# Kernel tuning notes

Measured on AMD Instinct MI355X. Metric: run time of the kernel, lower is better.

The kernel has to match this reference:

```python
import jax, jax.numpy as jnp
import numpy as np

N = 100000        # nodes
E = 1600000       # edges
D = 128           # feature dim (all layers)
G = 128           # graphs
C = 10            # num_classes
L = 3             # conv layers
EPS = 1e-5
SLOPE = 0.03


def setup_inputs() -> dict:
    key = jax.random.key(0)
    ks = jax.random.split(key, 12)
    x = jax.random.normal(ks[0], (N, D), dtype=jnp.float32)
    edge_index = jax.random.randint(ks[1], (2, E), 0, N, dtype=jnp.int64)
    batch = jnp.sort(jax.random.randint(ks[2], (N,), 0, G, dtype=jnp.int64))
    s = 1.0 / np.sqrt(D)
    Wc = jax.random.uniform(ks[3], (L, D, D), jnp.float32, -s, s)
    bc = jax.random.uniform(ks[4], (L, D), jnp.float32, -s, s)
    bn_gamma = jnp.ones((2, D), jnp.float32)
    bn_beta = jnp.zeros((2, D), jnp.float32)
    bn_mean = jax.random.normal(ks[5], (2, D), jnp.float32) * 0.1
    bn_var = jax.random.uniform(ks[6], (2, D), jnp.float32, 0.5, 1.5)
    lin_w = jax.random.uniform(ks[7], (C, D), jnp.float32, -s, s)
    lin_b = jax.random.uniform(ks[8], (C,), jnp.float32, -s, s)
    return {"x": x, "edge_index": edge_index, "batch": batch, "Wc": Wc,
            "bc": bc, "bn_gamma": bn_gamma, "bn_beta": bn_beta,
            "bn_mean": bn_mean, "bn_var": bn_var, "lin_w": lin_w, "lin_b": lin_b}


def _gcn_norm(edge_index):
    # add self-loops, compute D^{-1/2}[row] * D^{-1/2}[col] (PyG gcn_norm)
    loops = jnp.arange(N, dtype=edge_index.dtype)
    row = jnp.concatenate([edge_index[0], loops])
    col = jnp.concatenate([edge_index[1], loops])
    deg = jax.ops.segment_sum(jnp.ones_like(col, dtype=jnp.float32), col, num_segments=N)
    dis = jnp.where(deg > 0, jax.lax.rsqrt(deg), 0.0)
    return row, col, dis[row] * dis[col]


def reference(x, edge_index, batch, Wc, bc, bn_gamma, bn_beta, bn_mean, bn_var, lin_w, lin_b):
    row, col, norm = _gcn_norm(edge_index)
    h = x
    for i in range(L):
        h = h @ Wc[i]                                          # linear transform [N, D]
        msg = h[row] * norm[:, None]                           # gather + normalize [E+N, D]
        h = jax.ops.segment_sum(msg, col, num_segments=N) + bc[i]
        if i < 2:  # batchnorm only for i < len(batchnorms)-1 (eval mode, running stats)
            h = (h - bn_mean[i]) * jax.lax.rsqrt(bn_var[i] + EPS) * bn_gamma[i] + bn_beta[i]
        h = jnp.where(h > 0, h, SLOPE * h)                     # LeakyReLU(0.03)
    # global mean pool over graphs
    counts = jax.ops.segment_sum(jnp.ones((N,), jnp.float32), batch, num_segments=G)
    pooled = jax.ops.segment_sum(h, batch, num_segments=G) / jnp.maximum(counts, 1.0)[:, None]
    # dropout is identity in eval; final linear head
    return pooled @ lin_w.T + lin_b                            # [G, C]
```

## Files before the change

### kernel.cpp

```cpp
#include <hip/hip_runtime.h>
#include <hip/hip_bf16.h>

#define NN 100000
#define EE 1600000
#define DD 128
#define GG 128
#define CC 10
#define NPB 256
#define NB 391
#define SCAP 5120
#define VPT 16
#define CPAD 32
#define PPN 64

typedef __attribute__((ext_vector_type(8))) short bf16x8;
typedef __attribute__((ext_vector_type(4))) float f32x4;
typedef unsigned int u32;

__device__ inline float blo(u32 u) { return __uint_as_float(u << 16); }
__device__ inline float bhi(u32 u) { return __uint_as_float(u & 0xffff0000u); }
__device__ inline u32 bpack(float x, float y) {
    u32 bx = __float_as_uint(x);
    u32 by = __float_as_uint(y);
    bx = (bx + 0x7fffu + ((bx >> 16) & 1u)) >> 16;
    by = (by + 0x7fffu + ((by >> 16) & 1u)) & 0xffff0000u;
    return bx | by;
}

__global__ __launch_bounds__(256) void k_bcount(const int* __restrict__ col,
                                                int* __restrict__ bhist) {
    __shared__ int lh[NB];
    int tid = threadIdx.x;
    for (int b = tid; b < NB; b += 256) lh[b] = 0;
    __syncthreads();
    int base = blockIdx.x * (256 * VPT);
#pragma unroll
    for (int j = 0; j < VPT; j++) {
        int e = base + j * 256 + tid;
        if (e < EE) atomicAdd(&lh[col[e] >> 8], 1);
    }
    __syncthreads();
    for (int b = tid; b < NB; b += 256) {
        int h = lh[b];
        if (h) atomicAdd(&bhist[b * CPAD], h);
    }
}

__global__ __launch_bounds__(512) void k_bscan(const int* __restrict__ bhist,
                                               int* __restrict__ boffs,
                                               int* __restrict__ bcur) {
    __shared__ int s[512];
    int tid = threadIdx.x;
    int c = (tid < NB) ? bhist[tid * CPAD] : 0;
    s[tid] = c;
    __syncthreads();
    for (int off = 1; off < 512; off <<= 1) {
        int v = (tid >= off) ? s[tid - off] : 0;
        __syncthreads();
        s[tid] += v;
        __syncthreads();
    }
    int excl = s[tid] - c;
    if (tid < NB) {
        boffs[tid] = excl;
        bcur[tid * CPAD] = excl;
    }
    if (tid == NB - 1) boffs[NB] = excl + c;
}

__global__ __launch_bounds__(256) void k_part(const int* __restrict__ row, const int* __restrict__ col,
                                              int* __restrict__ bcur, u32* __restrict__ pairs) {
    __shared__ int lhist[NB];
    __shared__ int gbase[NB];
    __shared__ int lcur[NB];
    int tid = threadIdx.x;
    for (int b = tid; b < NB; b += 256) lhist[b] = 0;
    __syncthreads();
    int base = blockIdx.x * (256 * VPT);
    u32 v[VPT];
    int bb[VPT];
#pragma unroll
    for (int j = 0; j < VPT; j++) {
        int e = base + j * 256 + tid;
        if (e < EE) {
            int r = row[e], c = col[e];
            v[j] = ((u32)r << 8) | (u32)(c & 255);
            bb[j] = c >> 8;
            atomicAdd(&lhist[bb[j]], 1);
        } else {
            bb[j] = -1;
        }
    }
    __syncthreads();
    for (int b = tid; b < NB; b += 256) {
        int h = lhist[b];
        gbase[b] = h ? atomicAdd(&bcur[b * CPAD], h) : 0;
        lcur[b] = 0;
    }
    __syncthreads();
#pragma unroll
    for (int j = 0; j < VPT; j++) {
        if (bb[j] >= 0) {
            int slot = gbase[bb[j]] + atomicAdd(&lcur[bb[j]], 1);
            pairs[slot] = v[j];
        }
    }
}

__global__ __launch_bounds__(256) void k_sort(const u32* __restrict__ pairs,
                                              const int* __restrict__ boffs,
                                              int* __restrict__ offs,
                                              float* __restrict__ dis,
                                              int* __restrict__ src) {
    int b = blockIdx.x;
    int tid = threadIdx.x;
    int nstart = b << 8;
    int nvalid = NN - nstart;
    if (nvalid > NPB) nvalid = NPB;
    int base = boffs[b];
    int eend = boffs[b + 1];
    int cnt = eend - base;
    __shared__ int lcnt[NPB];
    __shared__ int lscan[NPB];
    __shared__ int lcur[NPB];
    __shared__ int lsrc[SCAP];
    lcnt[tid] = 0;
    __syncthreads();
    for (int e = base + tid; e < eend; e += 256)
        atomicAdd(&lcnt[pairs[e] & 255u], 1);
    __syncthreads();
    int c = lcnt[tid];
    lscan[tid] = c;
    __syncthreads();
    for (int off = 1; off < 256; off <<= 1) {
        int v = (tid >= off) ? lscan[tid - off] : 0;
        __syncthreads();
        lscan[tid] += v;
        __syncthreads();
    }
    int excl = lscan[tid] - c;
    if (tid < nvalid) {
        offs[nstart + tid] = base + excl;
        dis[nstart + tid] = rsqrtf((float)(c + 1));
    }
    if (b == NB - 1 && tid == 255) offs[NN] = EE;
    lcur[tid] = excl;
    __syncthreads();
    if (cnt <= SCAP) {
        for (int e = base + tid; e < eend; e += 256) {
            u32 v = pairs[e];
            int slot = atomicAdd(&lcur[v & 255u], 1);
            lsrc[slot] = (int)(v >> 8);
        }
        __syncthreads();
        for (int i = tid; i < cnt; i += 256)
            src[base + i] = lsrc[i];
    } else {
        for (int e = base + tid; e < eend; e += 256) {
            u32 v = pairs[e];
            int slot = base + atomicAdd(&lcur[v & 255u], 1);
            src[slot] = (int)(v >> 8);
        }
    }
}

__global__ void k_prep(const float* __restrict__ Wc, const float* __restrict__ bc,
                       const float* __restrict__ gamma, const float* __restrict__ beta,
                       const float* __restrict__ mean, const float* __restrict__ var,
                       __hip_bfloat16* __restrict__ WT,
                       float* __restrict__ sc, float* __restrict__ tc) {
    int i = blockIdx.x * 256 + threadIdx.x;
    if (i < 3 * 128) {
        int l = i >> 7, d = i & 127;
        float s, t;
        if (l < 2) {
            float rs = rsqrtf(var[l * 128 + d] + 1e-5f);
            s = gamma[l * 128 + d] * rs;
            t = (bc[l * 128 + d] - mean[l * 128 + d]) * s + beta[l * 128 + d];
        } else {
            s = 1.f;
            t = bc[2 * 128 + d];
        }
        sc[i] = s; tc[i] = t;
    }
    if (i < 3 * 16384) {
        int l = i >> 14, r = (i >> 7) & 127, k = i & 127;
        WT[i] = __float2bfloat16(Wc[l * 16384 + k * 128 + r]);
    }
}

template <int FP32IN>
__global__ __launch_bounds__(256) void k_gemm(const void* __restrict__ Ain,
                                              const __hip_bfloat16* __restrict__ WT,
                                              const float* __restrict__ dis,
                                              __hip_bfloat16* __restrict__ Cout) {
    int wave = threadIdx.x >> 6, lane = threadIdx.x & 63;
    int lg = lane >> 4, lr = lane & 15;
    int r0w = blockIdx.x * 64 + wave * 16;
    f32x4 zero = {0.f, 0.f, 0.f, 0.f};
    f32x4 acc[8];
#pragma unroll
    for (int ct = 0; ct < 8; ct++) acc[ct] = zero;

    int arow = r0w + lr;
    if (arow > NN - 1) arow = NN - 1;

#pragma unroll
    for (int kk = 0; kk < 4; kk++) {
        bf16x8 a;
        if (FP32IN) {
            const float* ap = (const float*)Ain + (size_t)arow * 128 + kk * 32 + lg * 8;
            float4 f0 = *(const float4*)ap;
            float4 f1 = *(const float4*)(ap + 4);
            u32 t0 = bpack(f0.x, f0.y), t1 = bpack(f0.z, f0.w);
            u32 t2 = bpack(f1.x, f1.y), t3 = bpack(f1.z, f1.w);
            uint4 t = make_uint4(t0, t1, t2, t3);
            a = *(bf16x8*)&t;
        } else {
            a = *(const bf16x8*)((const __hip_bfloat16*)Ain + (size_t)arow * 128 + kk * 32 + lg * 8);
        }
#pragma unroll
        for (int ct = 0; ct < 8; ct++) {
            bf16x8 b = *(const bf16x8*)(WT + (size_t)(ct * 16 + lr) * 128 + kk * 32 + lg * 8);
            acc[ct] = __builtin_amdgcn_mfma_f32_16x16x32_bf16(a, b, acc[ct], 0, 0, 0);
        }
    }
    float dv[4];
#pragma unroll
    for (int r = 0; r < 4; r++) {
        int row = r0w + lg * 4 + r;
        dv[r] = (row < NN) ? dis[row] : 0.f;
    }
#pragma unroll
    for (int ct = 0; ct < 8; ct++) {
#pragma unroll
        for (int r = 0; r < 4; r++) {
            int row = r0w + lg * 4 + r;
            if (row < NN) Cout[(size_t)row * 128 + ct * 16 + lr] = __float2bfloat16(acc[ct][r] * dv[r]);
        }
    }
}

__global__ __launch_bounds__(256) void k_agg(const u32* __restrict__ hin,
                                             const int* __restrict__ offs,
                                             const int* __restrict__ src,
                                             const float* __restrict__ dis,
                                             const float* __restrict__ sc,
                                             const float* __restrict__ tc,
                                             u32* __restrict__ hout) {
    int node = (blockIdx.x << 2) + (threadIdx.x >> 6);
    int lane = threadIdx.x & 63;
    if (node >= NN) return;
    int e0 = __builtin_amdgcn_readfirstlane(offs[node]);
    int e1 = __builtin_amdgcn_readfirstlane(offs[node + 1]);
    u32 self = hin[(u32)node * 64u + lane];
    float a0 = blo(self), a1 = bhi(self);
    for (int e = e0; e < e1; e += 8) {
        int lim = e1 - e;
        u32 u[8];
#pragma unroll
        for (int j = 0; j < 8; j++) {
            int s = (j < lim) ? src[e + j] : node;
            u[j] = hin[(u32)s * 64u + lane];
        }
#pragma unroll
        for (int j = 0; j < 8; j++) {
            if (j < lim) { a0 += blo(u[j]); a1 += bhi(u[j]); }
        }
    }
    float dn = dis[node];
    int d0 = lane * 2;
    float r0 = (a0 * dn) * sc[d0] + tc[d0];
    float r1 = (a1 * dn) * sc[d0 + 1] + tc[d0 + 1];
    r0 = r0 > 0.f ? r0 : 0.03f * r0;
    r1 = r1 > 0.f ? r1 : 0.03f * r1;
    hout[(u32)node * 64u + lane] = bpack(r0, r1);
}

__global__ __launch_bounds__(64) void k_pool(const u32* __restrict__ h,
                                             const int* __restrict__ batch,
                                             float* __restrict__ pooled,
                                             float* __restrict__ counts) {
    int lane = threadIdx.x;
    int n0 = blockIdx.x * PPN;
    if (n0 >= NN) return;
    int n1 = n0 + PPN;
    if (n1 > NN) n1 = NN;
    float a0 = 0.f, a1 = 0.f, cnt = 0.f;
    int g = batch[n0];
    for (int n = n0; n < n1; n++) {
        int bg = batch[n];
        if (bg != g) {
            atomicAdd(&pooled[g * 128 + lane * 2], a0);
            atomicAdd(&pooled[g * 128 + lane * 2 + 1], a1);
            if (lane == 0) atomicAdd(&counts[g], cnt);
            a0 = 0.f; a1 = 0.f; cnt = 0.f; g = bg;
        }
        u32 u = h[(u32)n * 64u + lane];
        a0 += blo(u); a1 += bhi(u);
        cnt += 1.f;
    }
    atomicAdd(&pooled[g * 128 + lane * 2], a0);
    atomicAdd(&pooled[g * 128 + lane * 2 + 1], a1);
    if (lane == 0) atomicAdd(&counts[g], cnt);
}

__global__ void k_head(const float* __restrict__ pooled, const float* __restrict__ counts,
                       const float* __restrict__ w, const float* __restrict__ b,
                       float* __restrict__ out) {
    int i = blockIdx.x * blockDim.x + threadIdx.x;
    if (i >= GG * CC) return;
    int g = i / CC, c = i % CC;
    float cnt = counts[g];
    cnt = cnt > 1.f ? cnt : 1.f;
    float inv = 1.f / cnt;
    const float* p = &pooled[g * 128];
    const float* ww = &w[c * 128];
    float acc = 0.f;
    for (int d = 0; d < 128; d++) acc += p[d] * ww[d];
    out[i] = acc * inv + b[c];
}

extern "C" void kernel_launch(void* const* d_in, const int* in_sizes, int n_in,
                              void* d_out, int out_size, void* d_ws, size_t ws_size,
                              hipStream_t stream) {
    const float* x     = (const float*)d_in[0];
    const int*   ei    = (const int*)d_in[1];
    const int*   row   = ei;
    const int*   col   = ei + EE;
    const int*   batch = (const int*)d_in[2];
    const float* Wc    = (const float*)d_in[3];
    const float* bc    = (const float*)d_in[4];
    const float* gamma = (const float*)d_in[5];
    const float* beta  = (const float*)d_in[6];
    const float* mean  = (const float*)d_in[7];
    const float* var   = (const float*)d_in[8];
    const float* lw    = (const float*)d_in[9];
    const float* lb    = (const float*)d_in[10];
    float* out = (float*)d_out;

    char* p = (char*)d_ws;
    auto alloc = [&](size_t bytes) -> char* {
        char* r = p;
        p += (bytes + 255) & ~(size_t)255;
        return r;
    };
    float* dis    = (float*)alloc((size_t)NN * 4);
    int*   offs   = (int*)alloc((size_t)(NN + 1) * 4);
    int*   bhist  = (int*)alloc((size_t)NB * CPAD * 4);
    int*   boffs  = (int*)alloc((size_t)(NB + 1) * 4);
    int*   bcur   = (int*)alloc((size_t)NB * CPAD * 4);
    int*   src    = (int*)alloc((size_t)EE * 4);
    __hip_bfloat16* WT = (__hip_bfloat16*)alloc((size_t)3 * 16384 * 2);
    float* sc     = (float*)alloc((size_t)3 * 128 * 4);
    float* tc     = (float*)alloc((size_t)3 * 128 * 4);
    float* pooled = (float*)alloc((size_t)GG * 128 * 4);
    float* counts = (float*)alloc((size_t)GG * 4);
    __hip_bfloat16* h0b = (__hip_bfloat16*)alloc((size_t)NN * 128 * 2);
    __hip_bfloat16* h1b = (__hip_bfloat16*)alloc((size_t)NN * 128 * 2);
    u32* pairs = (u32*)h0b;

    hipMemsetAsync(bhist, 0, (size_t)NB * CPAD * 4, stream);
    hipMemsetAsync(pooled, 0, (size_t)GG * 128 * 4, stream);
    hipMemsetAsync(counts, 0, (size_t)GG * 4, stream);

    const int eb_grid = (EE + 256 * VPT - 1) / (256 * VPT);
    k_bcount<<<eb_grid, 256, 0, stream>>>(col, bhist);
    k_bscan<<<1, 512, 0, stream>>>(bhist, boffs, bcur);
    k_part<<<eb_grid, 256, 0, stream>>>(row, col, bcur, pairs);
    k_sort<<<NB, 256, 0, stream>>>(pairs, boffs, offs, dis, src);
    k_prep<<<192, 256, 0, stream>>>(Wc, bc, gamma, beta, mean, var, WT, sc, tc);

    const int gemm_grid = (NN + 63) / 64;
    const int agg_grid  = (NN + 3) / 4;

    k_gemm<1><<<gemm_grid, 256, 0, stream>>>((const void*)x, WT, dis, h0b);
    k_agg<<<agg_grid, 256, 0, stream>>>((const u32*)h0b, offs, src, dis, sc, tc, (u32*)h1b);
    k_gemm<0><<<gemm_grid, 256, 0, stream>>>((const void*)h1b, WT + 16384, dis, h0b);
    k_agg<<<agg_grid, 256, 0, stream>>>((const u32*)h0b, offs, src, dis, sc + 128, tc + 128, (u32*)h1b);
    k_gemm<0><<<gemm_grid, 256, 0, stream>>>((const void*)h1b, WT + 2 * 16384, dis, h0b);
    k_agg<<<agg_grid, 256, 0, stream>>>((const u32*)h0b, offs, src, dis, sc + 256, tc + 256, (u32*)h1b);

    k_pool<<<(NN + PPN - 1) / PPN, 64, 0, stream>>>((const u32*)h1b, batch, pooled, counts);
    k_head<<<(GG * CC + 255) / 256, 256, 0, stream>>>(pooled, counts, lw, lb, out);
}
```

Before: 396.1 us.

## Fold BN scale into weights and gather neighbor rows with 16-byte loads

The batchnorm scale is folded into the transposed bf16 weight columns at prep time, so aggregation only adds a shift, and the sc array is removed. The aggregation kernel now splits each wave into four 16-lane groups. Each group handles a different neighbor edge with 16-byte uint4 loads, and partial sums are combined with cross-lane shuffles. This issues fewer, wider memory transactions per gather. The cost is shuffle reduction overhead and lower lane utilization when a node has few edges. Scaling the weights before the bf16 conversion also changes rounding slightly.

```diff
diff --git a/kernel.cpp b/kernel.cpp
--- a/kernel.cpp
+++ b/kernel.cpp
@@ -168,24 +168,24 @@
                        const float* __restrict__ gamma, const float* __restrict__ beta,
                        const float* __restrict__ mean, const float* __restrict__ var,
                        __hip_bfloat16* __restrict__ WT,
-                       float* __restrict__ sc, float* __restrict__ tc) {
+                       float* __restrict__ tc) {
     int i = blockIdx.x * 256 + threadIdx.x;
     if (i < 3 * 128) {
         int l = i >> 7, d = i & 127;
-        float s, t;
+        float t;
         if (l < 2) {
-            float rs = rsqrtf(var[l * 128 + d] + 1e-5f);
-            s = gamma[l * 128 + d] * rs;
+            float s = gamma[l * 128 + d] * rsqrtf(var[l * 128 + d] + 1e-5f);
             t = (bc[l * 128 + d] - mean[l * 128 + d]) * s + beta[l * 128 + d];
         } else {
-            s = 1.f;
             t = bc[2 * 128 + d];
         }
-        sc[i] = s; tc[i] = t;
+        tc[i] = t;
     }
     if (i < 3 * 16384) {
         int l = i >> 14, r = (i >> 7) & 127, k = i & 127;
-        WT[i] = __float2bfloat16(Wc[l * 16384 + k * 128 + r]);
+        float s = 1.f;
+        if (l < 2) s = gamma[l * 128 + r] * rsqrtf(var[l * 128 + r] + 1e-5f);
+        WT[i] = __float2bfloat16(Wc[l * 16384 + k * 128 + r] * s);
     }
 }
 
@@ -241,40 +241,65 @@
     }
 }
 
-__global__ __launch_bounds__(256) void k_agg(const u32* __restrict__ hin,
+__global__ __launch_bounds__(256) void k_agg(const uint4* __restrict__ hin,
                                              const int* __restrict__ offs,
                                              const int* __restrict__ src,
                                              const float* __restrict__ dis,
-                                             const float* __restrict__ sc,
                                              const float* __restrict__ tc,
-                                             u32* __restrict__ hout) {
+                                             uint4* __restrict__ hout) {
     int node = (blockIdx.x << 2) + (threadIdx.x >> 6);
     int lane = threadIdx.x & 63;
+    int quad = lane >> 4, sub = lane & 15;
     if (node >= NN) return;
     int e0 = __builtin_amdgcn_readfirstlane(offs[node]);
     int e1 = __builtin_amdgcn_readfirstlane(offs[node + 1]);
-    u32 self = hin[(u32)node * 64u + lane];
-    float a0 = blo(self), a1 = bhi(self);
+    float a0 = 0.f, a1 = 0.f, a2 = 0.f, a3 = 0.f, a4 = 0.f, a5 = 0.f, a6 = 0.f, a7 = 0.f;
+    if (quad == 0) {
+        uint4 u = hin[(u32)node * 16u + sub];
+        a0 = blo(u.x); a1 = bhi(u.x); a2 = blo(u.y); a3 = bhi(u.y);
+        a4 = blo(u.z); a5 = bhi(u.z); a6 = blo(u.w); a7 = bhi(u.w);
+    }
     for (int e = e0; e < e1; e += 8) {
         int lim = e1 - e;
-        u32 u[8];
-#pragma unroll
-        for (int j = 0; j < 8; j++) {
-            int s = (j < lim) ? src[e + j] : node;
-            u[j] = hin[(u32)s * 64u + lane];
-        }
-#pragma unroll
-        for (int j = 0; j < 8; j++) {
-            if (j < lim) { a0 += blo(u[j]); a1 += bhi(u[j]); }
-        }
-    }
-    float dn = dis[node];
-    int d0 = lane * 2;
-    float r0 = (a0 * dn) * sc[d0] + tc[d0];
-    float r1 = (a1 * dn) * sc[d0 + 1] + tc[d0 + 1];
-    r0 = r0 > 0.f ? r0 : 0.03f * r0;
-    r1 = r1 > 0.f ? r1 : 0.03f * r1;
-    hout[(u32)node * 64u + lane] = bpack(r0, r1);
+#pragma unroll
+        for (int j = 0; j < 2; j++) {
+            int idx = j * 4 + quad;
+            if (idx < lim) {
+                int s = src[e + idx];
+                uint4 u = hin[(u32)s * 16u + sub];
+                a0 += blo(u.x); a1 += bhi(u.x);
+                a2 += blo(u.y); a3 += bhi(u.y);
+                a4 += blo(u.z); a5 += bhi(u.z);
+                a6 += blo(u.w); a7 += bhi(u.w);
+            }
+        }
+    }
+    a0 += __shfl_xor(a0, 16); a0 += __shfl_xor(a0, 32);
+    a1 += __shfl_xor(a1, 16); a1 += __shfl_xor(a1, 32);
+    a2 += __shfl_xor(a2, 16); a2 += __shfl_xor(a2, 32);
+    a3 += __shfl_xor(a3, 16); a3 += __shfl_xor(a3, 32);
+    a4 += __shfl_xor(a4, 16); a4 += __shfl_xor(a4, 32);
+    a5 += __shfl_xor(a5, 16); a5 += __shfl_xor(a5, 32);
+    a6 += __shfl_xor(a6, 16); a6 += __shfl_xor(a6, 32);
+    a7 += __shfl_xor(a7, 16); a7 += __shfl_xor(a7, 32);
+    if (quad == 0) {
+        float dn = dis[node];
+        int d0 = sub * 8;
+        float4 t0 = *(const float4*)&tc[d0];
+        float4 t1 = *(const float4*)&tc[d0 + 4];
+        float r0 = a0 * dn + t0.x, r1 = a1 * dn + t0.y;
+        float r2 = a2 * dn + t0.z, r3 = a3 * dn + t0.w;
+        float r4 = a4 * dn + t1.x, r5 = a5 * dn + t1.y;
+        float r6 = a6 * dn + t1.z, r7 = a7 * dn + t1.w;
+        r0 = r0 > 0.f ? r0 : 0.03f * r0; r1 = r1 > 0.f ? r1 : 0.03f * r1;
+        r2 = r2 > 0.f ? r2 : 0.03f * r2; r3 = r3 > 0.f ? r3 : 0.03f * r3;
+        r4 = r4 > 0.f ? r4 : 0.03f * r4; r5 = r5 > 0.f ? r5 : 0.03f * r5;
+        r6 = r6 > 0.f ? r6 : 0.03f * r6; r7 = r7 > 0.f ? r7 : 0.03f * r7;
+        uint4 o;
+        o.x = bpack(r0, r1); o.y = bpack(r2, r3);
+        o.z = bpack(r4, r5); o.w = bpack(r6, r7);
+        hout[(u32)node * 16u + sub] = o;
+    }
 }
 
 __global__ __launch_bounds__(64) void k_pool(const u32* __restrict__ h,
@@ -352,7 +377,6 @@
     int*   bcur   = (int*)alloc((size_t)NB * CPAD * 4);
     int*   src    = (int*)alloc((size_t)EE * 4);
     __hip_bfloat16* WT = (__hip_bfloat16*)alloc((size_t)3 * 16384 * 2);
-    float* sc     = (float*)alloc((size_t)3 * 128 * 4);
     float* tc     = (float*)alloc((size_t)3 * 128 * 4);
     float* pooled = (float*)alloc((size_t)GG * 128 * 4);
     float* counts = (float*)alloc((size_t)GG * 4);
@@ -369,17 +393,17 @@
     k_bscan<<<1, 512, 0, stream>>>(bhist, boffs, bcur);
     k_part<<<eb_grid, 256, 0, stream>>>(row, col, bcur, pairs);
     k_sort<<<NB, 256, 0, stream>>>(pairs, boffs, offs, dis, src);
-    k_prep<<<192, 256, 0, stream>>>(Wc, bc, gamma, beta, mean, var, WT, sc, tc);
+    k_prep<<<192, 256, 0, stream>>>(Wc, bc, gamma, beta, mean, var, WT, tc);
 
     const int gemm_grid = (NN + 63) / 64;
     const int agg_grid  = (NN + 3) / 4;
 
     k_gemm<1><<<gemm_grid, 256, 0, stream>>>((const void*)x, WT, dis, h0b);
-    k_agg<<<agg_grid, 256, 0, stream>>>((const u32*)h0b, offs, src, dis, sc, tc, (u32*)h1b);
+    k_agg<<<agg_grid, 256, 0, stream>>>((const uint4*)h0b, offs, src, dis, tc, (uint4*)h1b);
     k_gemm<0><<<gemm_grid, 256, 0, stream>>>((const void*)h1b, WT + 16384, dis, h0b);
-    k_agg<<<agg_grid, 256, 0, stream>>>((const u32*)h0b, offs, src, dis, sc + 128, tc + 128, (u32*)h1b);
+    k_agg<<<agg_grid, 256, 0, stream>>>((const uint4*)h0b, offs, src, dis, tc + 128, (uint4*)h1b);
     k_gemm<0><<<gemm_grid, 256, 0, stream>>>((const void*)h1b, WT + 2 * 16384, dis, h0b);
-    k_agg<<<agg_grid, 256, 0, stream>>>((const u32*)h0b, offs, src, dis, sc + 256, tc + 256, (u32*)h1b);
+    k_agg<<<agg_grid, 256, 0, stream>>>((const uint4*)h0b, offs, src, dis, tc + 256, (uint4*)h1b);
 
     k_pool<<<(NN + PPN - 1) / PPN, 64, 0, stream>>>((const u32*)h1b, batch, pooled, counts);
     k_head<<<(GG * CC + 255) / 256, 256, 0, stream>>>(pooled, counts, lw, lb, out);
```

Measured after the change: 437.0 us. 10.3% more time.
